# Optimization experiments

Hardware: AMD Instinct MI355X
Metric: run time of the kernel (lower is better)

The kernel has to match this reference:

```python
import jax, jax.numpy as jnp
import numpy as np

NUM_ITER = 3
SLOT_DIM = 16
INPUT_DIM = 256
HIDDEN_DIM = 128
EPS = 1e-8
LN_EPS = 1e-5  # torch LayerNorm default


def _layernorm(x, w, b):
    mu = jnp.mean(x, axis=-1, keepdims=True)
    var = jnp.mean((x - mu) ** 2, axis=-1, keepdims=True)
    return (x - mu) * jax.lax.rsqrt(var + LN_EPS) * w + b


def setup_inputs() -> dict:
    key = jax.random.key(0)
    ks = jax.random.split(key, 12)
    B, N, K = 32, 4096, 8
    D, S, H = INPUT_DIM, SLOT_DIM, HIDDEN_DIM
    inputs = jax.random.normal(ks[0], (B, N, D), dtype=jnp.float32)
    init_slots = jax.random.normal(ks[1], (B, K, S), dtype=jnp.float32)
    return {
        "inputs": inputs,
        "init_slots": init_slots,
        "ln_in_w": jnp.ones((D,), jnp.float32),
        "ln_in_b": jnp.zeros((D,), jnp.float32),
        "ln_s_w": jnp.ones((S,), jnp.float32),
        "ln_s_b": jnp.zeros((S,), jnp.float32),
        "ln_m_w": jnp.ones((S,), jnp.float32),
        "ln_m_b": jnp.zeros((S,), jnp.float32),
        "wq": jax.random.normal(ks[2], (S, S), jnp.float32) * (S ** -0.5),
        "wk": jax.random.normal(ks[3], (S, D), jnp.float32) * (D ** -0.5),
        "wv": jax.random.normal(ks[4], (S, D), jnp.float32) * (D ** -0.5),
        "w_ih": jax.random.normal(ks[5], (3 * S, S), jnp.float32) * (S ** -0.5),
        "w_hh": jax.random.normal(ks[6], (3 * S, S), jnp.float32) * (S ** -0.5),
        "b_ih": jnp.zeros((3 * S,), jnp.float32),
        "b_hh": jnp.zeros((3 * S,), jnp.float32),
        "mlp_w1": jax.random.normal(ks[7], (H, S), jnp.float32) * (S ** -0.5),
        "mlp_b1": jnp.zeros((H,), jnp.float32),
        "mlp_w2": jax.random.normal(ks[8], (S, H), jnp.float32) * (H ** -0.5),
        "mlp_b2": jnp.zeros((S,), jnp.float32),
    }


def _gru_cell(x, h, w_ih, w_hh, b_ih, b_hh):
    # torch GRUCell: gates ordered [r, z, n]
    gi = x @ w_ih.T + b_ih            # [BK, 3S]
    gh = h @ w_hh.T + b_hh
    i_r, i_z, i_n = jnp.split(gi, 3, axis=-1)
    h_r, h_z, h_n = jnp.split(gh, 3, axis=-1)
    r = jax.nn.sigmoid(i_r + h_r)
    z = jax.nn.sigmoid(i_z + h_z)
    n = jnp.tanh(i_n + r * h_n)
    return (1.0 - z) * n + z * h


def reference(inputs, init_slots, ln_in_w, ln_in_b, ln_s_w, ln_s_b, ln_m_w, ln_m_b,
              wq, wk, wv, w_ih, w_hh, b_ih, b_hh, mlp_w1, mlp_b1, mlp_w2, mlp_b2):
    B, N, _ = inputs.shape
    K = init_slots.shape[1]
    scale = SLOT_DIM ** -0.5

    x = _layernorm(inputs, ln_in_w, ln_in_b)
    k = jnp.einsum('bnd,sd->bns', x, wk)   # [B,N,S]
    v = jnp.einsum('bnd,sd->bns', x, wv)

    slots = init_slots
    attn = None
    for _ in range(NUM_ITER):
        slots_prev = slots
        q = jnp.einsum('bks,ts->bkt', _layernorm(slots, ln_s_w, ln_s_b), wq)
        logits = jnp.einsum('bks,bns->bkn', q, k) * scale       # [B,K,N]
        attn = jax.nn.softmax(logits, axis=1) + EPS              # softmax over SLOTS
        attn = attn / jnp.sum(attn, axis=-1, keepdims=True)
        updates = jnp.einsum('bkn,bns->bks', attn, v)            # [B,K,S]
        h = _gru_cell(updates.reshape(B * K, -1), slots_prev.reshape(B * K, -1),
                      w_ih, w_hh, b_ih, b_hh).reshape(B, K, -1)
        y = _layernorm(h, ln_m_w, ln_m_b)
        mlp = jax.nn.relu(y @ mlp_w1.T + mlp_b1) @ mlp_w2.T + mlp_b2
        slots = h + mlp
    return slots, attn
```

## Files before the change

### kernel.cpp

```cpp
#include <hip/hip_runtime.h>
#include <cstddef>


typedef unsigned short ushort_t;
typedef __attribute__((ext_vector_type(8))) short short8;
typedef __attribute__((ext_vector_type(4))) float f32x4;

__device__ __forceinline__ float sigmoid_f(float x){ return 1.f/(1.f+__expf(-x)); }
__device__ __forceinline__ float tanh_f(float x){ return 1.f - 2.f/(__expf(2.f*x)+1.f); }

__device__ __forceinline__ ushort_t f2bf(float x){
  unsigned u = __float_as_uint(x);
  return (ushort_t)((u + 0x7FFFu + ((u>>16)&1u)) >> 16);
}
__device__ __forceinline__ float bf2f(ushort_t b){
  return __uint_as_float(((unsigned)b) << 16);
}

__global__ __launch_bounds__(256) void k_prep(
    const float* __restrict__ lnw, const float* __restrict__ lnb,
    const float* __restrict__ wk, const float* __restrict__ wv,
    const float* __restrict__ init_slots,
    const float* __restrict__ ln_s_w, const float* __restrict__ ln_s_b,
    const float* __restrict__ wq,
    ushort_t* __restrict__ Wh, ushort_t* __restrict__ Wl,
    float* __restrict__ mt,
    float* __restrict__ qbuf, float* __restrict__ upd, float* __restrict__ Abuf,
    float* __restrict__ slots_out)
{
  int t = threadIdx.x;
  int i = blockIdx.x*256 + t;
  {
    int s = i >> 8, d = i & 255;
    float w = (s < 16) ? wk[s*256+d] : wv[(s-16)*256+d];
    float w0 = lnw[d]*w;
    ushort_t hb = f2bf(w0);
    ushort_t lb = f2bf(w0 - bf2f(hb));
    Wh[i] = hb; Wl[i] = lb;
  }
  if (blockIdx.x != 0) return;
  {
    int s = t >> 3, j = t & 7;
    float m = 0.f, tv = 0.f;
    for (int d = j; d < 256; d += 8) {
      float w = (s < 16) ? wk[s*256+d] : wv[(s-16)*256+d];
      float w0 = lnw[d]*w;
      ushort_t hb = f2bf(w0);
      float hf = bf2f(hb);
      float lf = bf2f(f2bf(w0 - hf));
      m  += hf + lf;
      tv  = fmaf(lnb[d], w, tv);
    }
    m += __shfl_xor(m,1);  m += __shfl_xor(m,2);  m += __shfl_xor(m,4);
    tv += __shfl_xor(tv,1); tv += __shfl_xor(tv,2); tv += __shfl_xor(tv,4);
    if (j == 0) { mt[s] = m; mt[32+s] = tv; }
  }
  #pragma unroll
  for (int j2 = 0; j2 < 16; ++j2) {
    slots_out[t*16+j2] = init_slots[t*16+j2];
    upd[t*16+j2] = 0.f;
  }
  Abuf[t] = 0.f;
  float sl[16];
  #pragma unroll
  for (int j2 = 0; j2 < 16; ++j2) sl[j2] = init_slots[t*16+j2];
  float mu = 0.f;
  #pragma unroll
  for (int j2 = 0; j2 < 16; ++j2) mu += sl[j2];
  mu *= (1.f/16.f);
  float var = 0.f;
  #pragma unroll
  for (int j2 = 0; j2 < 16; ++j2) { float d = sl[j2]-mu; var = fmaf(d,d,var); }
  var *= (1.f/16.f);
  float rstd = rsqrtf(var + 1e-5f);
  float y[16];
  #pragma unroll
  for (int j2 = 0; j2 < 16; ++j2) y[j2] = (sl[j2]-mu)*rstd*ln_s_w[j2] + ln_s_b[j2];
  #pragma unroll
  for (int tq = 0; tq < 16; ++tq) {
    float q = 0.f;
    #pragma unroll
    for (int s2 = 0; s2 < 16; ++s2) q = fmaf(y[s2], wq[tq*16+s2], q);
    qbuf[t*16+tq] = q;
  }
}

__global__ __launch_bounds__(256, 4) void k_proj(
    const float* __restrict__ x, const ushort_t* __restrict__ Wh,
    const ushort_t* __restrict__ Wl, const float* __restrict__ mt,
    float* __restrict__ kout, float* __restrict__ vout)
{
  int t = threadIdx.x;
  int w = t >> 6, lane = t & 63;
  int m = lane & 15, quad = lane >> 4;
  int r0w = blockIdx.x*64 + w*16;
  const float* xr = x + (size_t)(r0w + m)*256 + quad*8;
  const ushort_t* wh0 = Wh + (size_t)m*256 + quad*8;
  const ushort_t* wh1 = wh0 + 16*256;
  const ushort_t* wl0 = Wl + (size_t)m*256 + quad*8;
  const ushort_t* wl1 = wl0 + 16*256;

  f32x4 acck = {0.f,0.f,0.f,0.f}, accv = {0.f,0.f,0.f,0.f};
  float sum = 0.f, sumsq = 0.f;

  #pragma unroll
  for (int kk = 0; kk < 8; ++kk) {
    float4 a0 = *(const float4*)(xr + kk*32);
    float4 a1 = *(const float4*)(xr + kk*32 + 4);
    short8 bh_k = *(const short8*)(wh0 + kk*32);
    short8 bh_v = *(const short8*)(wh1 + kk*32);
    short8 bl_k = *(const short8*)(wl0 + kk*32);
    short8 bl_v = *(const short8*)(wl1 + kk*32);
    float xv[8] = {a0.x,a0.y,a0.z,a0.w, a1.x,a1.y,a1.z,a1.w};
    short8 ah, al;
    #pragma unroll
    for (int j = 0; j < 8; ++j) {
      float v = xv[j];
      sum += v; sumsq = fmaf(v, v, sumsq);
      ushort_t hb = f2bf(v);
      ushort_t lb = f2bf(v - bf2f(hb));
      ah[j] = (short)hb; al[j] = (short)lb;
    }
    acck = __builtin_amdgcn_mfma_f32_16x16x32_bf16(ah, bh_k, acck, 0, 0, 0);
    accv = __builtin_amdgcn_mfma_f32_16x16x32_bf16(ah, bh_v, accv, 0, 0, 0);
    acck = __builtin_amdgcn_mfma_f32_16x16x32_bf16(al, bh_k, acck, 0, 0, 0);
    accv = __builtin_amdgcn_mfma_f32_16x16x32_bf16(al, bh_v, accv, 0, 0, 0);
    acck = __builtin_amdgcn_mfma_f32_16x16x32_bf16(ah, bl_k, acck, 0, 0, 0);
    accv = __builtin_amdgcn_mfma_f32_16x16x32_bf16(ah, bl_v, accv, 0, 0, 0);
  }

  sum   += __shfl_xor(sum, 16);  sum   += __shfl_xor(sum, 32);
  sumsq += __shfl_xor(sumsq, 16); sumsq += __shfl_xor(sumsq, 32);

  float mtk  = mt[m],    mtv  = mt[16+m];
  float mtkb = mt[32+m], mtvb = mt[48+m];
  #pragma unroll
  for (int r = 0; r < 4; ++r) {
    int row = quad*4 + r;
    float s_ = __shfl(sum,   row);
    float q_ = __shfl(sumsq, row);
    float mu = s_*(1.f/256.f);
    float var = q_*(1.f/256.f) - mu*mu;
    float rstd = rsqrtf(var + 1e-5f);
    float ok = fmaf(rstd, acck[r] - mu*mtk, mtkb);
    float ov = fmaf(rstd, accv[r] - mu*mtv, mtvb);
    kout[(size_t)(r0w + row)*16 + m] = ok;
    vout[(size_t)(r0w + row)*16 + m] = ov;
  }
}

__global__ __launch_bounds__(256) void k_attn(
    const float* __restrict__ kproj, const float* __restrict__ vproj,
    const float* __restrict__ qbuf,
    float* __restrict__ upd, float* __restrict__ Abuf,
    float* __restrict__ attn_out, int write_attn)
{
  __shared__ float qs[128];
  __shared__ float ktile[256*20];
  __shared__ float vtile[16*260];
  __shared__ float ptile[8*260];
  int b = blockIdx.x >> 4;
  int n0 = (blockIdx.x & 15) * 256;
  int t = threadIdx.x;

  const float* kbase = kproj + ((size_t)(b*4096 + n0))*16;
  const float* vbase = vproj + ((size_t)(b*4096 + n0))*16;
  {
    int nn = t >> 2, s0 = (t & 3)*4;
    #pragma unroll
    for (int i = 0; i < 4; ++i) {
      int n = i*64 + nn;
      float4 kf = *(const float4*)(kbase + n*16 + s0);
      *(float4*)&ktile[n*20 + s0] = kf;
      float4 vf = *(const float4*)(vbase + n*16 + s0);
      vtile[(s0+0)*260 + n] = vf.x;
      vtile[(s0+1)*260 + n] = vf.y;
      vtile[(s0+2)*260 + n] = vf.z;
      vtile[(s0+3)*260 + n] = vf.w;
    }
  }
  if (t < 128) qs[t] = qbuf[b*128 + t];
  __syncthreads();

  {
    float4 kv[4];
    #pragma unroll
    for (int i = 0; i < 4; ++i) kv[i] = *(const float4*)&ktile[t*20 + i*4];
    const float4* q4 = (const float4*)qs;
    float lg[8];
    #pragma unroll
    for (int kk = 0; kk < 8; ++kk) {
      float4 a4 = make_float4(0.f,0.f,0.f,0.f);
      #pragma unroll
      for (int i = 0; i < 4; ++i) {
        float4 q = q4[kk*4+i];
        a4.x = fmaf(q.x, kv[i].x, a4.x);
        a4.y = fmaf(q.y, kv[i].y, a4.y);
        a4.z = fmaf(q.z, kv[i].z, a4.z);
        a4.w = fmaf(q.w, kv[i].w, a4.w);
      }
      lg[kk] = ((a4.x+a4.y)+(a4.z+a4.w))*0.25f;
    }
    float mx = lg[0];
    #pragma unroll
    for (int kk = 1; kk < 8; ++kk) mx = fmaxf(mx, lg[kk]);
    float se = 0.f;
    #pragma unroll
    for (int kk = 0; kk < 8; ++kk) { lg[kk] = __expf(lg[kk]-mx); se += lg[kk]; }
    float inv = 1.f/se;
    #pragma unroll
    for (int kk = 0; kk < 8; ++kk) {
      float pv = fmaf(lg[kk], inv, 1e-8f);
      ptile[kk*260 + t] = pv;
      if (write_attn) attn_out[((size_t)(b*8+kk))*4096 + n0 + t] = pv;
    }
  }
  __syncthreads();
  {
    int kk = t >> 5, r = t & 31, s = r >> 1, half = r & 1;
    const float4* pr = (const float4*)(ptile + kk*260 + half*128);
    const float4* vr = (const float4*)(vtile + s*260 + half*128);
    float4 a4 = make_float4(0.f,0.f,0.f,0.f);
    float4 s4 = make_float4(0.f,0.f,0.f,0.f);
    #pragma unroll 8
    for (int i = 0; i < 32; ++i) {
      float4 pv = pr[i], vv = vr[i];
      s4.x += pv.x; s4.y += pv.y; s4.z += pv.z; s4.w += pv.w;
      a4.x = fmaf(pv.x, vv.x, a4.x);
      a4.y = fmaf(pv.y, vv.y, a4.y);
      a4.z = fmaf(pv.z, vv.z, a4.z);
      a4.w = fmaf(pv.w, vv.w, a4.w);
    }
    float acc  = (a4.x+a4.y)+(a4.z+a4.w);
    float asum = (s4.x+s4.y)+(s4.z+s4.w);
    acc  += __shfl_xor(acc, 1);
    asum += __shfl_xor(asum, 1);
    if (half == 0) {
      atomicAdd(upd + (b*8+kk)*16 + s, acc);
      if (s == 0) atomicAdd(Abuf + b*8 + kk, asum);
    }
  }
}

__global__ __launch_bounds__(256) void k_gru(
    float* __restrict__ upd, float* __restrict__ Abuf,
    float* __restrict__ slots, float* __restrict__ qbuf,
    const float* __restrict__ w_ih, const float* __restrict__ w_hh,
    const float* __restrict__ b_ih, const float* __restrict__ b_hh,
    const float* __restrict__ mlp_w1, const float* __restrict__ mlp_b1,
    const float* __restrict__ mlp_w2, const float* __restrict__ mlp_b2,
    const float* __restrict__ ln_m_w, const float* __restrict__ ln_m_b,
    const float* __restrict__ ln_s_w, const float* __restrict__ ln_s_b,
    const float* __restrict__ wq, int prep_next)
{
  __shared__ float s_wih[48*17], s_whh[48*17];
  __shared__ float s_bih[48], s_bhh[48];
  __shared__ float s_w1[128*17], s_b1[128];
  __shared__ float s_w2[16*129], s_b2[16];
  __shared__ float s_lnmw[16], s_lnmb[16], s_lnsw[16], s_lnsb[16];
  __shared__ float s_wq[16*17];
  int t = threadIdx.x;
  for (int i = t; i < 768; i += 256) {
    int g = i >> 4, j = i & 15;
    s_wih[g*17+j] = w_ih[i];
    s_whh[g*17+j] = w_hh[i];
  }
  for (int i = t; i < 2048; i += 256) {
    int r = i >> 4, c = i & 15;
    s_w1[r*17+c] = mlp_w1[i];
    int r2 = i >> 7, c2 = i & 127;
    s_w2[r2*129+c2] = mlp_w2[i];
  }
  if (t < 48) { s_bih[t] = b_ih[t]; s_bhh[t] = b_hh[t]; }
  if (t < 128) s_b1[t] = mlp_b1[t];
  if (t < 16) {
    s_b2[t] = mlp_b2[t];
    s_lnmw[t] = ln_m_w[t]; s_lnmb[t] = ln_m_b[t];
    s_lnsw[t] = ln_s_w[t]; s_lnsb[t] = ln_s_b[t];
  }
  for (int i = t; i < 256; i += 256) {
    int r = i >> 4, c = i & 15;
    s_wq[r*17+c] = wq[i];
  }
  __syncthreads();

  int bk = blockIdx.x*16 + (t >> 4);
  int s = t & 15;
  int laneBase = (t & 63) & ~15;

  float inv = 1.f / Abuf[bk];
  float u[16], h[16];
  #pragma unroll
  for (int j = 0; j < 16; ++j) {
    u[j] = upd[bk*16+j] * inv;
    h[j] = slots[bk*16+j];
  }
  float hs = slots[bk*16+s];

  float gir = s_bih[s],  giz = s_bih[16+s], gin = s_bih[32+s];
  float ghr = s_bhh[s],  ghz = s_bhh[16+s], ghn = s_bhh[32+s];
  #pragma unroll
  for (int j = 0; j < 16; ++j) {
    gir = fmaf(u[j], s_wih[s*17+j], gir);
    giz = fmaf(u[j], s_wih[(16+s)*17+j], giz);
    gin = fmaf(u[j], s_wih[(32+s)*17+j], gin);
    ghr = fmaf(h[j], s_whh[s*17+j], ghr);
    ghz = fmaf(h[j], s_whh[(16+s)*17+j], ghz);
    ghn = fmaf(h[j], s_whh[(32+s)*17+j], ghn);
  }
  float rr = sigmoid_f(gir + ghr);
  float zz = sigmoid_f(giz + ghz);
  float nn = tanh_f(gin + rr*ghn);
  float hn = (1.f-zz)*nn + zz*hs;

  float ssum = hn;
  #pragma unroll
  for (int m = 1; m < 16; m <<= 1) ssum += __shfl_xor(ssum, m);
  float mu = ssum*(1.f/16.f);
  float dv = hn - mu;
  float vs = dv*dv;
  #pragma unroll
  for (int m = 1; m < 16; m <<= 1) vs += __shfl_xor(vs, m);
  float rstd = rsqrtf(vs*(1.f/16.f) + 1e-5f);
  float y = dv*rstd*s_lnmw[s] + s_lnmb[s];

  float yv[16];
  #pragma unroll
  for (int j = 0; j < 16; ++j) yv[j] = __shfl(y, laneBase + j);

  float h1[8];
  #pragma unroll
  for (int i = 0; i < 8; ++i) {
    int jj = i*16 + s;
    float a = s_b1[jj];
    #pragma unroll
    for (int q = 0; q < 16; ++q) a = fmaf(yv[q], s_w1[jj*17+q], a);
    h1[i] = fmaxf(a, 0.f);
  }
  float o = s_b2[s];
  #pragma unroll
  for (int i = 0; i < 8; ++i) {
    #pragma unroll
    for (int sp = 0; sp < 16; ++sp) {
      float hv = __shfl(h1[i], laneBase + sp);
      o = fmaf(hv, s_w2[s*129 + i*16 + sp], o);
    }
  }
  float slot_new = hn + o;
  slots[bk*16+s] = slot_new;

  if (prep_next) {
    float ss = slot_new;
    #pragma unroll
    for (int m = 1; m < 16; m <<= 1) ss += __shfl_xor(ss, m);
    float mu2 = ss*(1.f/16.f);
    float d2 = slot_new - mu2;
    float v2 = d2*d2;
    #pragma unroll
    for (int m = 1; m < 16; m <<= 1) v2 += __shfl_xor(v2, m);
    float rstd2 = rsqrtf(v2*(1.f/16.f) + 1e-5f);
    float y2 = d2*rstd2*s_lnsw[s] + s_lnsb[s];
    float qv = 0.f;
    #pragma unroll
    for (int sp = 0; sp < 16; ++sp) qv = fmaf(__shfl(y2, laneBase+sp), s_wq[s*17+sp], qv);
    qbuf[bk*16+s] = qv;
    upd[bk*16+s] = 0.f;
    if (s == 0) Abuf[bk] = 0.f;
  }
}

__global__ __launch_bounds__(256) void k_scale(float* __restrict__ attn,
                                               const float* __restrict__ Abuf)
{
  int bk = blockIdx.x;
  float inv = 1.f / Abuf[bk];
  float4* p = (float4*)(attn + (size_t)bk*4096);
  #pragma unroll 4
  for (int i = threadIdx.x; i < 1024; i += 256) {
    float4 v = p[i];
    v.x *= inv; v.y *= inv; v.z *= inv; v.w *= inv;
    p[i] = v;
  }
}

extern "C" void kernel_launch(void* const* d_in, const int* in_sizes, int n_in,
                              void* d_out, int out_size, void* d_ws, size_t ws_size,
                              hipStream_t stream)
{
  const float* inputs     = (const float*)d_in[0];
  const float* init_slots = (const float*)d_in[1];
  const float* ln_in_w    = (const float*)d_in[2];
  const float* ln_in_b    = (const float*)d_in[3];
  const float* ln_s_w     = (const float*)d_in[4];
  const float* ln_s_b     = (const float*)d_in[5];
  const float* ln_m_w     = (const float*)d_in[6];
  const float* ln_m_b     = (const float*)d_in[7];
  const float* wq         = (const float*)d_in[8];
  const float* wk         = (const float*)d_in[9];
  const float* wv         = (const float*)d_in[10];
  const float* w_ih       = (const float*)d_in[11];
  const float* w_hh       = (const float*)d_in[12];
  const float* b_ih       = (const float*)d_in[13];
  const float* b_hh       = (const float*)d_in[14];
  const float* mlp_w1     = (const float*)d_in[15];
  const float* mlp_b1     = (const float*)d_in[16];
  const float* mlp_w2     = (const float*)d_in[17];
  const float* mlp_b2     = (const float*)d_in[18];

  float* ws    = (float*)d_ws;
  ushort_t* Wh = (ushort_t*)ws;
  ushort_t* Wl = (ushort_t*)(ws + 4096);
  float* mt    = ws + 8192;
  float* qbuf  = ws + 8320;
  float* upd   = ws + 12416;
  float* Abuf  = ws + 16512;
  float* kproj = ws + 16768;
  float* vproj = kproj + 2097152;

  float* out   = (float*)d_out;
  float* slots = out;
  float* attn  = out + 4096;

  k_prep<<<32, 256, 0, stream>>>(ln_in_w, ln_in_b, wk, wv, init_slots,
                                 ln_s_w, ln_s_b, wq,
                                 Wh, Wl, mt, qbuf, upd, Abuf, slots);
  k_proj<<<2048, 256, 0, stream>>>(inputs, Wh, Wl, mt, kproj, vproj);
  for (int it = 0; it < 3; ++it) {
    int last = (it == 2);
    k_attn<<<512, 256, 0, stream>>>(kproj, vproj, qbuf, upd, Abuf, attn, last);
    k_gru<<<16, 256, 0, stream>>>(upd, Abuf, slots, qbuf,
                                  w_ih, w_hh, b_ih, b_hh,
                                  mlp_w1, mlp_b1, mlp_w2, mlp_b2,
                                  ln_m_w, ln_m_b, ln_s_w, ln_s_b,
                                  wq, last ? 0 : 1);
  }
  k_scale<<<256, 256, 0, stream>>>(attn, Abuf);
}
```

Measured before the change: 302.9 us.

## Fuse GRU into attention via last-block counter and stage proj inputs through LDS

The GRU/MLP slot update is folded into the attention kernel. The last block to finish, detected with an atomic counter, runs the update for all 256 slots, which removes three kernel launches and their gaps. The projection kernel now streams input rows into double-buffered, swizzled LDS using global_load_lds. Its bf16 hi/lo split switches from round-to-nearest to truncation, which is cheaper to compute. The tail work becomes serialized in a single block, the LDS footprint of the attention kernel grows, and the truncated split slightly changes numerics.

```diff
diff --git a/kernel.cpp b/kernel.cpp
--- a/kernel.cpp
+++ b/kernel.cpp
@@ -15,6 +15,13 @@
 }
 __device__ __forceinline__ float bf2f(ushort_t b){
   return __uint_as_float(((unsigned)b) << 16);
+}
+
+__device__ __forceinline__ void load16_to_lds(const float* g, float* l) {
+  __builtin_amdgcn_global_load_lds(
+      (const __attribute__((address_space(1))) unsigned int*)g,
+      (__attribute__((address_space(3))) unsigned int*)l,
+      16, 0, 0);
 }
 
 __global__ __launch_bounds__(256) void k_prep(
@@ -26,7 +33,7 @@
     ushort_t* __restrict__ Wh, ushort_t* __restrict__ Wl,
     float* __restrict__ mt,
     float* __restrict__ qbuf, float* __restrict__ upd, float* __restrict__ Abuf,
-    float* __restrict__ slots_out)
+    float* __restrict__ slots_out, unsigned* __restrict__ cnt)
 {
   int t = threadIdx.x;
   int i = blockIdx.x*256 + t;
@@ -39,6 +46,7 @@
     Wh[i] = hb; Wl[i] = lb;
   }
   if (blockIdx.x != 0) return;
+  if (t < 3) cnt[t] = 0;
   {
     int s = t >> 3, j = t & 7;
     float m = 0.f, tv = 0.f;
@@ -90,44 +98,75 @@
     const ushort_t* __restrict__ Wl, const float* __restrict__ mt,
     float* __restrict__ kout, float* __restrict__ vout)
 {
+  __shared__ float xs[2][64*64];
   int t = threadIdx.x;
-  int w = t >> 6, lane = t & 63;
+  int lane = t & 63;
+  int p = __builtin_amdgcn_readfirstlane(t >> 6);
   int m = lane & 15, quad = lane >> 4;
-  int r0w = blockIdx.x*64 + w*16;
-  const float* xr = x + (size_t)(r0w + m)*256 + quad*8;
-  const ushort_t* wh0 = Wh + (size_t)m*256 + quad*8;
-  const ushort_t* wh1 = wh0 + 16*256;
-  const ushort_t* wl0 = Wl + (size_t)m*256 + quad*8;
-  const ushort_t* wl1 = wl0 + 16*256;
+  int r0 = blockIdx.x*64;
+  const float* xbase = x + (size_t)r0*256;
+
+  int sr = lane >> 4;
+  int slot = lane & 15;
+  int row_st0 = p*16 + sr;
+  int cb0 = (slot - row_st0) & 15;
+
+  const ushort_t* whk = Wh + (size_t)m*256 + quad*8;
+  const ushort_t* whv = whk + 16*256;
+  const ushort_t* wlk = Wl + (size_t)m*256 + quad*8;
+  const ushort_t* wlv = wlk + 16*256;
+
+  #define ISSUE_CHUNK(c_, buf_)                                              \
+    _Pragma("unroll")                                                        \
+    for (int i = 0; i < 4; ++i) {                                            \
+      int row = row_st0 + i*4;                                               \
+      int cb  = (cb0 - i*4) & 15;                                            \
+      load16_to_lds(xbase + (size_t)row*256 + (c_)*64 + cb*4,                \
+                    &xs[buf_][(p*16 + i*4)*64]);                             \
+    }
 
   f32x4 acck = {0.f,0.f,0.f,0.f}, accv = {0.f,0.f,0.f,0.f};
   float sum = 0.f, sumsq = 0.f;
 
-  #pragma unroll
-  for (int kk = 0; kk < 8; ++kk) {
-    float4 a0 = *(const float4*)(xr + kk*32);
-    float4 a1 = *(const float4*)(xr + kk*32 + 4);
-    short8 bh_k = *(const short8*)(wh0 + kk*32);
-    short8 bh_v = *(const short8*)(wh1 + kk*32);
-    short8 bl_k = *(const short8*)(wl0 + kk*32);
-    short8 bl_v = *(const short8*)(wl1 + kk*32);
-    float xv[8] = {a0.x,a0.y,a0.z,a0.w, a1.x,a1.y,a1.z,a1.w};
-    short8 ah, al;
-    #pragma unroll
-    for (int j = 0; j < 8; ++j) {
-      float v = xv[j];
-      sum += v; sumsq = fmaf(v, v, sumsq);
-      ushort_t hb = f2bf(v);
-      ushort_t lb = f2bf(v - bf2f(hb));
-      ah[j] = (short)hb; al[j] = (short)lb;
-    }
-    acck = __builtin_amdgcn_mfma_f32_16x16x32_bf16(ah, bh_k, acck, 0, 0, 0);
-    accv = __builtin_amdgcn_mfma_f32_16x16x32_bf16(ah, bh_v, accv, 0, 0, 0);
-    acck = __builtin_amdgcn_mfma_f32_16x16x32_bf16(al, bh_k, acck, 0, 0, 0);
-    accv = __builtin_amdgcn_mfma_f32_16x16x32_bf16(al, bh_v, accv, 0, 0, 0);
-    acck = __builtin_amdgcn_mfma_f32_16x16x32_bf16(ah, bl_k, acck, 0, 0, 0);
-    accv = __builtin_amdgcn_mfma_f32_16x16x32_bf16(ah, bl_v, accv, 0, 0, 0);
-  }
+  ISSUE_CHUNK(0, 0)
+  __syncthreads();
+
+  int rowA = p*16 + m;
+  #pragma unroll 1
+  for (int c = 0; c < 4; ++c) {
+    if (c < 3) { ISSUE_CHUNK(c+1, (c+1)&1) }
+    const float* xb = xs[c&1];
+    #pragma unroll
+    for (int ks = 0; ks < 2; ++ks) {
+      int kk = c*2 + ks;
+      short8 bh_k = *(const short8*)(whk + kk*32);
+      short8 bh_v = *(const short8*)(whv + kk*32);
+      short8 bl_k = *(const short8*)(wlk + kk*32);
+      short8 bl_v = *(const short8*)(wlv + kk*32);
+      int cbA = ks*8 + quad*2;
+      float4 f0 = *(const float4*)&xb[rowA*64 + (((cbA  ) + m) & 15)*4];
+      float4 f1 = *(const float4*)&xb[rowA*64 + (((cbA+1) + m) & 15)*4];
+      float xv[8] = {f0.x,f0.y,f0.z,f0.w, f1.x,f1.y,f1.z,f1.w};
+      short8 ah, al;
+      #pragma unroll
+      for (int j = 0; j < 8; ++j) {
+        float v = xv[j];
+        sum += v; sumsq = fmaf(v, v, sumsq);
+        unsigned u = __float_as_uint(v);
+        ah[j] = (short)(u >> 16);
+        float hf = __uint_as_float(u & 0xFFFF0000u);
+        al[j] = (short)(__float_as_uint(v - hf) >> 16);
+      }
+      acck = __builtin_amdgcn_mfma_f32_16x16x32_bf16(ah, bh_k, acck, 0, 0, 0);
+      accv = __builtin_amdgcn_mfma_f32_16x16x32_bf16(ah, bh_v, accv, 0, 0, 0);
+      acck = __builtin_amdgcn_mfma_f32_16x16x32_bf16(al, bh_k, acck, 0, 0, 0);
+      accv = __builtin_amdgcn_mfma_f32_16x16x32_bf16(al, bh_v, accv, 0, 0, 0);
+      acck = __builtin_amdgcn_mfma_f32_16x16x32_bf16(ah, bl_k, acck, 0, 0, 0);
+      accv = __builtin_amdgcn_mfma_f32_16x16x32_bf16(ah, bl_v, accv, 0, 0, 0);
+    }
+    __syncthreads();
+  }
+  #undef ISSUE_CHUNK
 
   sum   += __shfl_xor(sum, 16);  sum   += __shfl_xor(sum, 32);
   sumsq += __shfl_xor(sumsq, 16); sumsq += __shfl_xor(sumsq, 32);
@@ -137,28 +176,46 @@
   #pragma unroll
   for (int r = 0; r < 4; ++r) {
     int row = quad*4 + r;
-    float s_ = __shfl(sum,   row);
+    float s_ = __shfl(sum,   p*0 + row);
     float q_ = __shfl(sumsq, row);
     float mu = s_*(1.f/256.f);
     float var = q_*(1.f/256.f) - mu*mu;
     float rstd = rsqrtf(var + 1e-5f);
     float ok = fmaf(rstd, acck[r] - mu*mtk, mtkb);
     float ov = fmaf(rstd, accv[r] - mu*mtv, mtvb);
-    kout[(size_t)(r0w + row)*16 + m] = ok;
-    vout[(size_t)(r0w + row)*16 + m] = ov;
-  }
-}
-
-__global__ __launch_bounds__(256) void k_attn(
+    size_t grow = (size_t)(r0 + p*16 + row)*16 + m;
+    kout[grow] = ok;
+    vout[grow] = ov;
+  }
+}
+
+__global__ __launch_bounds__(256) void k_attn_gru(
     const float* __restrict__ kproj, const float* __restrict__ vproj,
-    const float* __restrict__ qbuf,
+    const float* __restrict__ qbuf_in,
     float* __restrict__ upd, float* __restrict__ Abuf,
-    float* __restrict__ attn_out, int write_attn)
+    float* __restrict__ attn_out, int write_attn,
+    unsigned* __restrict__ cnt,
+    float* __restrict__ slots, float* __restrict__ qbuf_out,
+    const float* __restrict__ w_ih, const float* __restrict__ w_hh,
+    const float* __restrict__ b_ih, const float* __restrict__ b_hh,
+    const float* __restrict__ mlp_w1, const float* __restrict__ mlp_b1,
+    const float* __restrict__ mlp_w2, const float* __restrict__ mlp_b2,
+    const float* __restrict__ ln_m_w, const float* __restrict__ ln_m_b,
+    const float* __restrict__ ln_s_w, const float* __restrict__ ln_s_b,
+    const float* __restrict__ wq, int prep_next)
 {
   __shared__ float qs[128];
   __shared__ float ktile[256*20];
   __shared__ float vtile[16*260];
   __shared__ float ptile[8*260];
+  __shared__ float s_wih[48*17], s_whh[48*17];
+  __shared__ float s_bih[48], s_bhh[48];
+  __shared__ float s_w1[128*17], s_b1[128];
+  __shared__ float s_w2[16*129], s_b2[16];
+  __shared__ float s_lnmw[16], s_lnmb[16], s_lnsw[16], s_lnsb[16];
+  __shared__ float s_wq[16*17];
+  __shared__ unsigned s_last;
+
   int b = blockIdx.x >> 4;
   int n0 = (blockIdx.x & 15) * 256;
   int t = threadIdx.x;
@@ -179,7 +236,7 @@
       vtile[(s0+3)*260 + n] = vf.w;
     }
   }
-  if (t < 128) qs[t] = qbuf[b*128 + t];
+  if (t < 128) qs[t] = qbuf_in[b*128 + t];
   __syncthreads();
 
   {
@@ -240,26 +297,16 @@
       if (s == 0) atomicAdd(Abuf + b*8 + kk, asum);
     }
   }
-}
-
-__global__ __launch_bounds__(256) void k_gru(
-    float* __restrict__ upd, float* __restrict__ Abuf,
-    float* __restrict__ slots, float* __restrict__ qbuf,
-    const float* __restrict__ w_ih, const float* __restrict__ w_hh,
-    const float* __restrict__ b_ih, const float* __restrict__ b_hh,
-    const float* __restrict__ mlp_w1, const float* __restrict__ mlp_b1,
-    const float* __restrict__ mlp_w2, const float* __restrict__ mlp_b2,
-    const float* __restrict__ ln_m_w, const float* __restrict__ ln_m_b,
-    const float* __restrict__ ln_s_w, const float* __restrict__ ln_s_b,
-    const float* __restrict__ wq, int prep_next)
-{
-  __shared__ float s_wih[48*17], s_whh[48*17];
-  __shared__ float s_bih[48], s_bhh[48];
-  __shared__ float s_w1[128*17], s_b1[128];
-  __shared__ float s_w2[16*129], s_b2[16];
-  __shared__ float s_lnmw[16], s_lnmb[16], s_lnsw[16], s_lnsb[16];
-  __shared__ float s_wq[16*17];
-  int t = threadIdx.x;
+  __syncthreads();
+  if (t == 0) {
+    __threadfence();
+    unsigned old = __hip_atomic_fetch_add(cnt, 1u, __ATOMIC_ACQ_REL,
+                                          __HIP_MEMORY_SCOPE_AGENT);
+    s_last = (old == gridDim.x - 1) ? 1u : 0u;
+  }
+  __syncthreads();
+  if (!s_last) return;
+
   for (int i = t; i < 768; i += 256) {
     int g = i >> 4, j = i & 15;
     s_wih[g*17+j] = w_ih[i];
@@ -284,88 +331,94 @@
   }
   __syncthreads();
 
-  int bk = blockIdx.x*16 + (t >> 4);
   int s = t & 15;
   int laneBase = (t & 63) & ~15;
-
-  float inv = 1.f / Abuf[bk];
-  float u[16], h[16];
-  #pragma unroll
-  for (int j = 0; j < 16; ++j) {
-    u[j] = upd[bk*16+j] * inv;
-    h[j] = slots[bk*16+j];
-  }
-  float hs = slots[bk*16+s];
-
-  float gir = s_bih[s],  giz = s_bih[16+s], gin = s_bih[32+s];
-  float ghr = s_bhh[s],  ghz = s_bhh[16+s], ghn = s_bhh[32+s];
-  #pragma unroll
-  for (int j = 0; j < 16; ++j) {
-    gir = fmaf(u[j], s_wih[s*17+j], gir);
-    giz = fmaf(u[j], s_wih[(16+s)*17+j], giz);
-    gin = fmaf(u[j], s_wih[(32+s)*17+j], gin);
-    ghr = fmaf(h[j], s_whh[s*17+j], ghr);
-    ghz = fmaf(h[j], s_whh[(16+s)*17+j], ghz);
-    ghn = fmaf(h[j], s_whh[(32+s)*17+j], ghn);
-  }
-  float rr = sigmoid_f(gir + ghr);
-  float zz = sigmoid_f(giz + ghz);
-  float nn = tanh_f(gin + rr*ghn);
-  float hn = (1.f-zz)*nn + zz*hs;
-
-  float ssum = hn;
-  #pragma unroll
-  for (int m = 1; m < 16; m <<= 1) ssum += __shfl_xor(ssum, m);
-  float mu = ssum*(1.f/16.f);
-  float dv = hn - mu;
-  float vs = dv*dv;
-  #pragma unroll
-  for (int m = 1; m < 16; m <<= 1) vs += __shfl_xor(vs, m);
-  float rstd = rsqrtf(vs*(1.f/16.f) + 1e-5f);
-  float y = dv*rstd*s_lnmw[s] + s_lnmb[s];
-
-  float yv[16];
-  #pragma unroll
-  for (int j = 0; j < 16; ++j) yv[j] = __shfl(y, laneBase + j);
-
-  float h1[8];
-  #pragma unroll
-  for (int i = 0; i < 8; ++i) {
-    int jj = i*16 + s;
-    float a = s_b1[jj];
-    #pragma unroll
-    for (int q = 0; q < 16; ++q) a = fmaf(yv[q], s_w1[jj*17+q], a);
-    h1[i] = fmaxf(a, 0.f);
-  }
-  float o = s_b2[s];
-  #pragma unroll
-  for (int i = 0; i < 8; ++i) {
-    #pragma unroll
-    for (int sp = 0; sp < 16; ++sp) {
-      float hv = __shfl(h1[i], laneBase + sp);
-      o = fmaf(hv, s_w2[s*129 + i*16 + sp], o);
-    }
-  }
-  float slot_new = hn + o;
-  slots[bk*16+s] = slot_new;
-
-  if (prep_next) {
-    float ss = slot_new;
-    #pragma unroll
-    for (int m = 1; m < 16; m <<= 1) ss += __shfl_xor(ss, m);
-    float mu2 = ss*(1.f/16.f);
-    float d2 = slot_new - mu2;
-    float v2 = d2*d2;
-    #pragma unroll
-    for (int m = 1; m < 16; m <<= 1) v2 += __shfl_xor(v2, m);
-    float rstd2 = rsqrtf(v2*(1.f/16.f) + 1e-5f);
-    float y2 = d2*rstd2*s_lnsw[s] + s_lnsb[s];
-    float qv = 0.f;
-    #pragma unroll
-    for (int sp = 0; sp < 16; ++sp) qv = fmaf(__shfl(y2, laneBase+sp), s_wq[s*17+sp], qv);
-    qbuf[bk*16+s] = qv;
-    upd[bk*16+s] = 0.f;
-    if (s == 0) Abuf[bk] = 0.f;
+  #pragma unroll 1
+  for (int ch = 0; ch < 16; ++ch) {
+    int bk = ch*16 + (t >> 4);
+    float Aval = __hip_atomic_load(&Abuf[bk], __ATOMIC_RELAXED,
+                                   __HIP_MEMORY_SCOPE_AGENT);
+    float inv = 1.f / Aval;
+    float u[16], h[16];
+    #pragma unroll
+    for (int j = 0; j < 16; ++j) {
+      u[j] = __hip_atomic_load(&upd[bk*16+j], __ATOMIC_RELAXED,
+                               __HIP_MEMORY_SCOPE_AGENT) * inv;
+      h[j] = slots[bk*16+j];
+    }
+    float hs = slots[bk*16+s];
+
+    float gir = s_bih[s],  giz = s_bih[16+s], gin = s_bih[32+s];
+    float ghr = s_bhh[s],  ghz = s_bhh[16+s], ghn = s_bhh[32+s];
+    #pragma unroll
+    for (int j = 0; j < 16; ++j) {
+      gir = fmaf(u[j], s_wih[s*17+j], gir);
+      giz = fmaf(u[j], s_wih[(16+s)*17+j], giz);
+      gin = fmaf(u[j], s_wih[(32+s)*17+j], gin);
+      ghr = fmaf(h[j], s_whh[s*17+j], ghr);
+      ghz = fmaf(h[j], s_whh[(16+s)*17+j], ghz);
+      ghn = fmaf(h[j], s_whh[(32+s)*17+j], ghn);
+    }
+    float rr = sigmoid_f(gir + ghr);
+    float zz = sigmoid_f(giz + ghz);
+    float nn = tanh_f(gin + rr*ghn);
+    float hn = (1.f-zz)*nn + zz*hs;
+
+    float ssum = hn;
+    #pragma unroll
+    for (int mm = 1; mm < 16; mm <<= 1) ssum += __shfl_xor(ssum, mm);
+    float mu = ssum*(1.f/16.f);
+    float dv = hn - mu;
+    float vs = dv*dv;
+    #pragma unroll
+    for (int mm = 1; mm < 16; mm <<= 1) vs += __shfl_xor(vs, mm);
+    float rstd = rsqrtf(vs*(1.f/16.f) + 1e-5f);
+    float y = dv*rstd*s_lnmw[s] + s_lnmb[s];
+
+    float yv[16];
+    #pragma unroll
+    for (int j = 0; j < 16; ++j) yv[j] = __shfl(y, laneBase + j);
+
+    float h1[8];
+    #pragma unroll
+    for (int i = 0; i < 8; ++i) {
+      int jj = i*16 + s;
+      float a = s_b1[jj];
+      #pragma unroll
+      for (int q = 0; q < 16; ++q) a = fmaf(yv[q], s_w1[jj*17+q], a);
+      h1[i] = fmaxf(a, 0.f);
+    }
+    float o = s_b2[s];
+    #pragma unroll
+    for (int i = 0; i < 8; ++i) {
+      #pragma unroll
+      for (int sp = 0; sp < 16; ++sp) {
+        float hv = __shfl(h1[i], laneBase + sp);
+        o = fmaf(hv, s_w2[s*129 + i*16 + sp], o);
+      }
+    }
+    float slot_new = hn + o;
+    slots[bk*16+s] = slot_new;
+
+    if (prep_next) {
+      float ss = slot_new;
+      #pragma unroll
+      for (int mm = 1; mm < 16; mm <<= 1) ss += __shfl_xor(ss, mm);
+      float mu2 = ss*(1.f/16.f);
+      float d2 = slot_new - mu2;
+      float v2 = d2*d2;
+      #pragma unroll
+      for (int mm = 1; mm < 16; mm <<= 1) v2 += __shfl_xor(v2, mm);
+      float rstd2 = rsqrtf(v2*(1.f/16.f) + 1e-5f);
+      float y2 = d2*rstd2*s_lnsw[s] + s_lnsb[s];
+      float qv = 0.f;
+      #pragma unroll
+      for (int sp = 0; sp < 16; ++sp)
+        qv = fmaf(__shfl(y2, laneBase+sp), s_wq[s*17+sp], qv);
+      qbuf_out[bk*16+s] = qv;
+      upd[bk*16+s] = 0.f;
+      if (s == 0) Abuf[bk] = 0.f;
+    }
   }
 }
 
@@ -416,6 +469,7 @@
   float* Abuf  = ws + 16512;
   float* kproj = ws + 16768;
   float* vproj = kproj + 2097152;
+  unsigned* cnt = (unsigned*)(vproj + 2097152);
 
   float* out   = (float*)d_out;
   float* slots = out;
@@ -423,16 +477,17 @@
 
   k_prep<<<32, 256, 0, stream>>>(ln_in_w, ln_in_b, wk, wv, init_slots,
                                  ln_s_w, ln_s_b, wq,
-                                 Wh, Wl, mt, qbuf, upd, Abuf, slots);
+                                 Wh, Wl, mt, qbuf, upd, Abuf, slots, cnt);
   k_proj<<<2048, 256, 0, stream>>>(inputs, Wh, Wl, mt, kproj, vproj);
   for (int it = 0; it < 3; ++it) {
     int last = (it == 2);
-    k_attn<<<512, 256, 0, stream>>>(kproj, vproj, qbuf, upd, Abuf, attn, last);
-    k_gru<<<16, 256, 0, stream>>>(upd, Abuf, slots, qbuf,
-                                  w_ih, w_hh, b_ih, b_hh,
-                                  mlp_w1, mlp_b1, mlp_w2, mlp_b2,
-                                  ln_m_w, ln_m_b, ln_s_w, ln_s_b,
-                                  wq, last ? 0 : 1);
+    k_attn_gru<<<512, 256, 0, stream>>>(kproj, vproj, qbuf,
+                                        upd, Abuf, attn, last, &cnt[it],
+                                        slots, qbuf,
+                                        w_ih, w_hh, b_ih, b_hh,
+                                        mlp_w1, mlp_b1, mlp_w2, mlp_b2,
+                                        ln_m_w, ln_m_b, ln_s_w, ln_s_b,
+                                        wq, last ? 0 : 1);
   }
   k_scale<<<256, 256, 0, stream>>>(attn, Abuf);
 }
```

Measured after the change: 686.6 us. +126.7%, slower.
